# Kernel optimization log

Hardware: AMD Instinct MI355X
Metric: run time of the kernel (lower is better)

Reference implementation:

```python
import jax, jax.numpy as jnp
import numpy as np

B, T, C, H, D = 128, 256, 384, 6, 64  # batch, seq (block_size), embed, heads, head_size


def setup_inputs() -> dict:
    key = jax.random.key(0)
    ks = jax.random.split(key, 6)
    s = 0.02  # init scale
    return {
        "x": jax.random.normal(ks[0], (B, T, C), dtype=jnp.float32),
        "wq": jax.random.normal(ks[1], (H, C, D), dtype=jnp.float32) * s,
        "wk": jax.random.normal(ks[2], (H, C, D), dtype=jnp.float32) * s,
        "wv": jax.random.normal(ks[3], (H, C, D), dtype=jnp.float32) * s,
        "wp": jax.random.normal(ks[4], (H * D, C), dtype=jnp.float32) * s,
        "bp": jax.random.normal(ks[5], (C,), dtype=jnp.float32) * s,
    }


def reference(x, wq, wk, wv, wp, bp):
    # Batched multi-head causal self-attention (eval mode: dropout = identity).
    Bx, Tx, Cx = x.shape
    q = jnp.einsum("btc,hcd->bhtd", x, wq)
    k = jnp.einsum("btc,hcd->bhtd", x, wk)
    v = jnp.einsum("btc,hcd->bhtd", x, wv)
    scale = jnp.asarray(D, x.dtype) ** -0.5
    scores = jnp.einsum("bhtd,bhsd->bhts", q, k) * scale
    mask = jnp.tril(jnp.ones((Tx, Tx), dtype=bool))  # causal
    scores = jnp.where(mask, scores, -jnp.inf)
    w = jax.nn.softmax(scores, axis=-1)
    out = jnp.einsum("bhts,bhsd->bhtd", w, v)
    out = out.transpose(0, 2, 1, 3).reshape(Bx, Tx, H * D)  # concat heads
    return out @ wp + bp
```

## Files before the change

kernel.cpp:

```cpp
#include <hip/hip_runtime.h>
#include <hip/hip_bf16.h>

typedef __bf16 bf16x8 __attribute__((ext_vector_type(8)));
typedef __bf16 bf16x4 __attribute__((ext_vector_type(4)));
typedef float  f32x4  __attribute__((ext_vector_type(4)));

#define MFMA16(a,b,c) __builtin_amdgcn_mfma_f32_16x16x32_bf16((a),(b),(c),0,0,0)

static constexpr int Tt = 256;
static constexpr int Cc = 384;
static constexpr int Hh = 6;
static constexpr int Dd = 64;
static constexpr int HD = 384;
static constexpr int NQ = 1152;

__global__ __launch_bounds__(256) void prep_w(
    const float* __restrict__ wq, const float* __restrict__ wk,
    const float* __restrict__ wv, const float* __restrict__ wp,
    __bf16* __restrict__ wqkvb, __bf16* __restrict__ wpb)
{
  int idx = blockIdx.x * 256 + threadIdx.x;
  const int n1 = NQ * Cc;
  if (idx < n1) {
    int n = idx / Cc, c = idx % Cc;
    int which = n / HD, r = n % HD, h = r >> 6, d = r & 63;
    const float* w = which == 0 ? wq : (which == 1 ? wk : wv);
    wqkvb[idx] = (__bf16)w[(h * Cc + c) * Dd + d];
  } else {
    int j = idx - n1;
    if (j < Cc * HD) {
      int co = j / HD, ci = j % HD;
      wpb[j] = (__bf16)wp[ci * Cc + co];
    }
  }
}

__global__ __launch_bounds__(256) void gemm_qkv(
    const float* __restrict__ x, const __bf16* __restrict__ wn,
    __bf16* __restrict__ qkv, int Mc)
{
  __shared__ __align__(16) char smem[36864];
  __bf16* Al = (__bf16*)smem;
  __bf16* Bl = (__bf16*)(smem + 18432);

  const int tid = threadIdx.x;
  const int m0 = blockIdx.x * 128;
  const int n0 = blockIdx.y * 128;
  const int wid = tid >> 6, lane = tid & 63;
  const int wm = wid >> 1, wn_ = wid & 1;
  const int lr = lane & 15, lg = lane >> 4;

  f32x4 acc[4][4];
#pragma unroll
  for (int i = 0; i < 4; ++i)
#pragma unroll
    for (int j = 0; j < 4; ++j) acc[i][j] = f32x4{0.f, 0.f, 0.f, 0.f};

  for (int kt = 0; kt < Cc; kt += 64) {
#pragma unroll
    for (int i = 0; i < 8; ++i) {
      int idx = tid + 256 * i;
      int row = idx >> 4, c4 = idx & 15;
      float4 v = *(const float4*)(x + (size_t)(m0 + row) * Cc + kt + c4 * 4);
      bf16x4 b; b[0] = (__bf16)v.x; b[1] = (__bf16)v.y; b[2] = (__bf16)v.z; b[3] = (__bf16)v.w;
      *(bf16x4*)((char*)Al + row * 144 + c4 * 8) = b;
    }
#pragma unroll
    for (int i = 0; i < 4; ++i) {
      int idx = tid + 256 * i;
      int row = idx >> 3, k8 = idx & 7;
      bf16x8 v = *(const bf16x8*)(wn + (size_t)(n0 + row) * Cc + kt + k8 * 8);
      *(bf16x8*)((char*)Bl + row * 144 + k8 * 16) = v;
    }
    __syncthreads();
#pragma unroll
    for (int ks = 0; ks < 2; ++ks) {
      bf16x8 af[4], bfr[4];
#pragma unroll
      for (int mi = 0; mi < 4; ++mi)
        af[mi] = *(const bf16x8*)((char*)Al + (wm * 64 + mi * 16 + lr) * 144 + ks * 64 + lg * 16);
#pragma unroll
      for (int ni = 0; ni < 4; ++ni)
        bfr[ni] = *(const bf16x8*)((char*)Bl + (wn_ * 64 + ni * 16 + lr) * 144 + ks * 64 + lg * 16);
#pragma unroll
      for (int mi = 0; mi < 4; ++mi)
#pragma unroll
        for (int ni = 0; ni < 4; ++ni)
          acc[mi][ni] = MFMA16(af[mi], bfr[ni], acc[mi][ni]);
    }
    __syncthreads();
  }

  __bf16* Cl = (__bf16*)smem;
#pragma unroll
  for (int mi = 0; mi < 4; ++mi)
#pragma unroll
    for (int ni = 0; ni < 4; ++ni)
#pragma unroll
      for (int j = 0; j < 4; ++j) {
        int row = wm * 64 + mi * 16 + lg * 4 + j;
        int col = wn_ * 64 + ni * 16 + lr;
        *((__bf16*)((char*)Cl + row * 272 + col * 2)) = (__bf16)acc[mi][ni][j];
      }
  __syncthreads();
#pragma unroll
  for (int p = 0; p < 8; ++p) {
    int row = p * 16 + (tid >> 4);
    int ch = tid & 15;
    bf16x8 v = *(const bf16x8*)((char*)Cl + row * 272 + ch * 16);
    int m = m0 + row, n = n0 + ch * 8;
    int which = n / HD, r = n % HD, h = r >> 6, d = r & 63;
    int bl = m >> 8, t = m & 255;
    *(bf16x8*)(qkv + (size_t)which * ((size_t)Mc * HD) +
               ((size_t)(bl * Hh + h) * Tt + t) * Dd + d) = v;
  }
}

__global__ __launch_bounds__(256) void attn_k(
    const __bf16* __restrict__ q, const __bf16* __restrict__ k,
    const __bf16* __restrict__ v, __bf16* __restrict__ att)
{
  __shared__ __align__(16) char smem[98304];
  char* Kl = smem;
  char* Vl = smem + 32768;
  char* Pl = smem + 65536;

  const int bh = blockIdx.x;
  const int tid = threadIdx.x, wid = tid >> 6, lane = tid & 63;
  const int lr = lane & 15, lg = lane >> 4;
  const size_t base = (size_t)bh * (Tt * Dd);

#pragma unroll
  for (int i = 0; i < 8; ++i) {
    int chunk = tid + 256 * i;
    int key = chunk >> 3, d8 = chunk & 7;
    bf16x8 kv = *(const bf16x8*)(k + base + key * 64 + d8 * 8);
    *(bf16x8*)(Kl + ((key * 128 + d8 * 16) ^ ((key & 7) << 4))) = kv;
  }
#pragma unroll
  for (int i = 0; i < 8; ++i) {
    int chunk = tid + 256 * i;
    int key = chunk >> 3, d8 = chunk & 7;
    bf16x8 vv = *(const bf16x8*)(v + base + key * 64 + d8 * 8);
#pragma unroll
    for (int e = 0; e < 8; ++e) {
      int d = d8 * 8 + e;
      *(__bf16*)(Vl + ((d * 512 + key * 2) ^ ((d & 7) << 4))) = vv[e];
    }
  }
  __syncthreads();

  char* Pw = Pl + wid * 8192;
  const int bl = bh / Hh, h = bh % Hh;

  for (int qi = 0; qi < 4; ++qi) {
    const int qt = wid + qi * 4;
    const int qbase = qt * 16;

    bf16x8 qf0 = *(const bf16x8*)(q + base + (qbase + lr) * 64 + lg * 8);
    bf16x8 qf1 = *(const bf16x8*)(q + base + (qbase + lr) * 64 + 32 + lg * 8);

    f32x4 s[16];
#pragma unroll
    for (int n = 0; n < 16; ++n) s[n] = f32x4{0.f, 0.f, 0.f, 0.f};
#pragma unroll
    for (int n = 0; n < 16; ++n) {
      if (n <= qt) {
        int rowb = (n * 16 + lr) * 128;
        int swz = (lr & 7) << 4;
        bf16x8 k0 = *(const bf16x8*)(Kl + ((rowb + lg * 16) ^ swz));
        bf16x8 k1 = *(const bf16x8*)(Kl + ((rowb + 64 + lg * 16) ^ swz));
        s[n] = MFMA16(qf0, k0, s[n]);
        s[n] = MFMA16(qf1, k1, s[n]);
      }
    }
#pragma unroll
    for (int n = 0; n < 16; ++n)
#pragma unroll
      for (int j = 0; j < 4; ++j) {
        int key = n * 16 + lr;
        int qrow = qbase + lg * 4 + j;
        s[n][j] = (n <= qt && key <= qrow) ? s[n][j] * 0.125f : -1e30f;
      }
    float m4[4] = {-1e30f, -1e30f, -1e30f, -1e30f};
#pragma unroll
    for (int n = 0; n < 16; ++n)
#pragma unroll
      for (int j = 0; j < 4; ++j) m4[j] = fmaxf(m4[j], s[n][j]);
#pragma unroll
    for (int j = 0; j < 4; ++j) {
      m4[j] = fmaxf(m4[j], __shfl_xor(m4[j], 1));
      m4[j] = fmaxf(m4[j], __shfl_xor(m4[j], 2));
      m4[j] = fmaxf(m4[j], __shfl_xor(m4[j], 4));
      m4[j] = fmaxf(m4[j], __shfl_xor(m4[j], 8));
    }
    float sum4[4] = {0.f, 0.f, 0.f, 0.f};
#pragma unroll
    for (int n = 0; n < 16; ++n)
#pragma unroll
      for (int j = 0; j < 4; ++j) {
        float p = __expf(s[n][j] - m4[j]);
        s[n][j] = p;
        sum4[j] += p;
      }
#pragma unroll
    for (int j = 0; j < 4; ++j) {
      sum4[j] += __shfl_xor(sum4[j], 1);
      sum4[j] += __shfl_xor(sum4[j], 2);
      sum4[j] += __shfl_xor(sum4[j], 4);
      sum4[j] += __shfl_xor(sum4[j], 8);
    }
    float inv4[4];
#pragma unroll
    for (int j = 0; j < 4; ++j) inv4[j] = 1.0f / sum4[j];

#pragma unroll
    for (int j = 0; j < 4; ++j) {
      int ql = lg * 4 + j;
      int rswz = (ql & 7) << 4;
#pragma unroll
      for (int n = 0; n < 16; ++n) {
        float p = s[n][j] * inv4[j];
        *(__bf16*)(Pw + ((ql * 512 + (n * 16 + lr) * 2) ^ rswz)) = (__bf16)p;
      }
    }
    asm volatile("s_waitcnt lgkmcnt(0)" ::: "memory");

    f32x4 o[4];
#pragma unroll
    for (int dn = 0; dn < 4; ++dn) o[dn] = f32x4{0.f, 0.f, 0.f, 0.f};
    const int kkmax = (qbase + 15) >> 5;
#pragma unroll
    for (int kk = 0; kk < 8; ++kk) {
      if (kk <= kkmax) {
        bf16x8 pa = *(const bf16x8*)(Pw + ((lr * 512 + kk * 64 + lg * 16) ^ ((lr & 7) << 4)));
#pragma unroll
        for (int dn = 0; dn < 4; ++dn) {
          int d = dn * 16 + lr;
          bf16x8 vb = *(const bf16x8*)(Vl + ((d * 512 + kk * 64 + lg * 16) ^ ((d & 7) << 4)));
          o[dn] = MFMA16(pa, vb, o[dn]);
        }
      }
    }
#pragma unroll
    for (int dn = 0; dn < 4; ++dn)
#pragma unroll
      for (int j = 0; j < 4; ++j) {
        int qrow = qbase + lg * 4 + j;
        att[((size_t)(bl * Tt + qrow)) * HD + h * Dd + dn * 16 + lr] = (__bf16)o[dn][j];
      }
  }
}

__global__ __launch_bounds__(256) void gemm_out(
    const __bf16* __restrict__ att, const __bf16* __restrict__ wpb,
    const float* __restrict__ bp, float* __restrict__ out, int Mc)
{
  __shared__ __align__(16) char smem[36864];
  __bf16* Al = (__bf16*)smem;
  __bf16* Bl = (__bf16*)(smem + 18432);

  const int tid = threadIdx.x;
  const int m0 = blockIdx.x * 128;
  const int n0 = blockIdx.y * 128;
  const int wid = tid >> 6, lane = tid & 63;
  const int wm = wid >> 1, wn_ = wid & 1;
  const int lr = lane & 15, lg = lane >> 4;

  f32x4 acc[4][4];
#pragma unroll
  for (int i = 0; i < 4; ++i)
#pragma unroll
    for (int j = 0; j < 4; ++j) acc[i][j] = f32x4{0.f, 0.f, 0.f, 0.f};

  for (int kt = 0; kt < Cc; kt += 64) {
#pragma unroll
    for (int i = 0; i < 4; ++i) {
      int idx = tid + 256 * i;
      int row = idx >> 3, k8 = idx & 7;
      bf16x8 v = *(const bf16x8*)(att + (size_t)(m0 + row) * Cc + kt + k8 * 8);
      *(bf16x8*)((char*)Al + row * 144 + k8 * 16) = v;
    }
#pragma unroll
    for (int i = 0; i < 4; ++i) {
      int idx = tid + 256 * i;
      int row = idx >> 3, k8 = idx & 7;
      bf16x8 v = *(const bf16x8*)(wpb + (size_t)(n0 + row) * Cc + kt + k8 * 8);
      *(bf16x8*)((char*)Bl + row * 144 + k8 * 16) = v;
    }
    __syncthreads();
#pragma unroll
    for (int ks = 0; ks < 2; ++ks) {
      bf16x8 af[4], bfr[4];
#pragma unroll
      for (int mi = 0; mi < 4; ++mi)
        af[mi] = *(const bf16x8*)((char*)Al + (wm * 64 + mi * 16 + lr) * 144 + ks * 64 + lg * 16);
#pragma unroll
      for (int ni = 0; ni < 4; ++ni)
        bfr[ni] = *(const bf16x8*)((char*)Bl + (wn_ * 64 + ni * 16 + lr) * 144 + ks * 64 + lg * 16);
#pragma unroll
      for (int mi = 0; mi < 4; ++mi)
#pragma unroll
        for (int ni = 0; ni < 4; ++ni)
          acc[mi][ni] = MFMA16(af[mi], bfr[ni], acc[mi][ni]);
    }
    __syncthreads();
  }
#pragma unroll
  for (int ni = 0; ni < 4; ++ni) {
    int n = n0 + wn_ * 64 + ni * 16 + lr;
    float bv = bp[n];
#pragma unroll
    for (int mi = 0; mi < 4; ++mi)
#pragma unroll
      for (int j = 0; j < 4; ++j) {
        int m = m0 + wm * 64 + mi * 16 + lg * 4 + j;
        out[(size_t)m * Cc + n] = acc[mi][ni][j] + bv;
      }
  }
}

extern "C" void kernel_launch(void* const* d_in, const int* in_sizes, int n_in,
                              void* d_out, int out_size, void* d_ws, size_t ws_size,
                              hipStream_t stream) {
  const float* x  = (const float*)d_in[0];
  const float* wq = (const float*)d_in[1];
  const float* wk = (const float*)d_in[2];
  const float* wv = (const float*)d_in[3];
  const float* wp = (const float*)d_in[4];
  const float* bp = (const float*)d_in[5];
  float* out = (float*)d_out;

  char* ws = (char*)d_ws;
  __bf16* wqkvb = (__bf16*)ws;
  __bf16* wpb   = (__bf16*)(ws + 884736);
  char*   dyn   = ws + 1179648;

  int Bc = 128;
  while (Bc > 1 && 1179648ull + (unsigned long long)Bc * 786432ull > (unsigned long long)ws_size)
    Bc >>= 1;
  const int Mc = Bc * 256;
  __bf16* qkv = (__bf16*)dyn;
  __bf16* att = (__bf16*)(dyn + (size_t)3 * Mc * HD * 2);

  prep_w<<<2304, 256, 0, stream>>>(wq, wk, wv, wp, wqkvb, wpb);

  for (int b0 = 0; b0 < 128; b0 += Bc) {
    const float* xc  = x + (size_t)b0 * Tt * Cc;
    float* outc      = out + (size_t)b0 * Tt * Cc;
    gemm_qkv<<<dim3(Mc / 128, 9), 256, 0, stream>>>(xc, wqkvb, qkv, Mc);
    attn_k<<<Bc * Hh, 256, 0, stream>>>(qkv, qkv + (size_t)Mc * HD,
                                        qkv + (size_t)2 * Mc * HD, att);
    gemm_out<<<dim3(Mc / 128, 3), 256, 0, stream>>>(att, wpb, bp, outc, Mc);
  }
}
```

Baseline: 253.6 us.

## Use direct global-to-LDS loads, pre-cast x, widen attention blocks to 512 threads

Adds a separate kernel that casts x to bf16 once, so both GEMMs can stage tiles with global_load_lds into XOR-swizzled LDS in place of padded register round-trips. Attention now runs 8 waves per block with balanced causal query-tile pairing (wid and 15-wid), and loads K via direct LDS loads. s_setprio brackets the MFMA sections. The xb buffer is aliased with att to save workspace. This adds an extra kernel launch and a bf16 round-trip of x through memory, and raises LDS use in attention to 128 KB.

```diff
diff --git a/kernel.cpp b/kernel.cpp
--- a/kernel.cpp
+++ b/kernel.cpp
@@ -13,6 +13,24 @@
 static constexpr int Dd = 64;
 static constexpr int HD = 384;
 static constexpr int NQ = 1152;
+
+__device__ __forceinline__ void gload16(const void* g, void* l) {
+  __builtin_amdgcn_global_load_lds(
+      (const __attribute__((address_space(1))) void*)g,
+      (__attribute__((address_space(3))) void*)l, 16, 0, 0);
+}
+
+__global__ __launch_bounds__(256) void xcast(
+    const float* __restrict__ x, __bf16* __restrict__ xb)
+{
+  size_t i = (size_t)blockIdx.x * 256 + threadIdx.x;
+  const float4* p = (const float4*)(x + i * 8);
+  float4 a = p[0], b = p[1];
+  bf16x8 o;
+  o[0] = (__bf16)a.x; o[1] = (__bf16)a.y; o[2] = (__bf16)a.z; o[3] = (__bf16)a.w;
+  o[4] = (__bf16)b.x; o[5] = (__bf16)b.y; o[6] = (__bf16)b.z; o[7] = (__bf16)b.w;
+  *(bf16x8*)(xb + i * 8) = o;
+}
 
 __global__ __launch_bounds__(256) void prep_w(
     const float* __restrict__ wq, const float* __restrict__ wk,
@@ -36,19 +54,20 @@
 }
 
 __global__ __launch_bounds__(256) void gemm_qkv(
-    const float* __restrict__ x, const __bf16* __restrict__ wn,
+    const __bf16* __restrict__ xb, const __bf16* __restrict__ wn,
     __bf16* __restrict__ qkv, int Mc)
 {
   __shared__ __align__(16) char smem[36864];
-  __bf16* Al = (__bf16*)smem;
-  __bf16* Bl = (__bf16*)(smem + 18432);
+  char* Al = smem;
+  char* Bl = smem + 16384;
 
   const int tid = threadIdx.x;
   const int m0 = blockIdx.x * 128;
   const int n0 = blockIdx.y * 128;
-  const int wid = tid >> 6, lane = tid & 63;
+  const int wid = tid >> 6, ln = tid & 63;
   const int wm = wid >> 1, wn_ = wid & 1;
-  const int lr = lane & 15, lg = lane >> 4;
+  const int lr = ln & 15, lg = ln >> 4;
+  const int srow = ln >> 3, sslot = ln & 7;
 
   f32x4 acc[4][4];
 #pragma unroll
@@ -58,35 +77,38 @@
 
   for (int kt = 0; kt < Cc; kt += 64) {
 #pragma unroll
-    for (int i = 0; i < 8; ++i) {
-      int idx = tid + 256 * i;
-      int row = idx >> 4, c4 = idx & 15;
-      float4 v = *(const float4*)(x + (size_t)(m0 + row) * Cc + kt + c4 * 4);
-      bf16x4 b; b[0] = (__bf16)v.x; b[1] = (__bf16)v.y; b[2] = (__bf16)v.z; b[3] = (__bf16)v.w;
-      *(bf16x4*)((char*)Al + row * 144 + c4 * 8) = b;
-    }
-#pragma unroll
     for (int i = 0; i < 4; ++i) {
-      int idx = tid + 256 * i;
-      int row = idx >> 3, k8 = idx & 7;
-      bf16x8 v = *(const bf16x8*)(wn + (size_t)(n0 + row) * Cc + kt + k8 * 8);
-      *(bf16x8*)((char*)Bl + row * 144 + k8 * 16) = v;
+      int off = (wid * 4 + i) << 10;
+      int row = (off >> 7) + srow;
+      gload16(xb + (size_t)(m0 + row) * Cc + kt + ((sslot ^ (row & 7)) << 3), Al + off);
+    }
+#pragma unroll
+    for (int i = 0; i < 4; ++i) {
+      int off = (wid * 4 + i) << 10;
+      int row = (off >> 7) + srow;
+      gload16(wn + (size_t)(n0 + row) * Cc + kt + ((sslot ^ (row & 7)) << 3), Bl + off);
     }
     __syncthreads();
 #pragma unroll
     for (int ks = 0; ks < 2; ++ks) {
       bf16x8 af[4], bfr[4];
 #pragma unroll
-      for (int mi = 0; mi < 4; ++mi)
-        af[mi] = *(const bf16x8*)((char*)Al + (wm * 64 + mi * 16 + lr) * 144 + ks * 64 + lg * 16);
-#pragma unroll
-      for (int ni = 0; ni < 4; ++ni)
-        bfr[ni] = *(const bf16x8*)((char*)Bl + (wn_ * 64 + ni * 16 + lr) * 144 + ks * 64 + lg * 16);
+      for (int mi = 0; mi < 4; ++mi) {
+        int r = wm * 64 + mi * 16 + lr;
+        af[mi] = *(const bf16x8*)(Al + r * 128 + (((ks * 4 + lg) ^ (r & 7)) << 4));
+      }
+#pragma unroll
+      for (int ni = 0; ni < 4; ++ni) {
+        int r = wn_ * 64 + ni * 16 + lr;
+        bfr[ni] = *(const bf16x8*)(Bl + r * 128 + (((ks * 4 + lg) ^ (r & 7)) << 4));
+      }
+      __builtin_amdgcn_s_setprio(1);
 #pragma unroll
       for (int mi = 0; mi < 4; ++mi)
 #pragma unroll
         for (int ni = 0; ni < 4; ++ni)
           acc[mi][ni] = MFMA16(af[mi], bfr[ni], acc[mi][ni]);
+      __builtin_amdgcn_s_setprio(0);
     }
     __syncthreads();
   }
@@ -116,11 +138,11 @@
   }
 }
 
-__global__ __launch_bounds__(256) void attn_k(
+__global__ __launch_bounds__(512) void attn_k(
     const __bf16* __restrict__ q, const __bf16* __restrict__ k,
     const __bf16* __restrict__ v, __bf16* __restrict__ att)
 {
-  __shared__ __align__(16) char smem[98304];
+  __shared__ __align__(16) char smem[131072];
   char* Kl = smem;
   char* Vl = smem + 32768;
   char* Pl = smem + 65536;
@@ -131,15 +153,15 @@
   const size_t base = (size_t)bh * (Tt * Dd);
 
 #pragma unroll
-  for (int i = 0; i < 8; ++i) {
-    int chunk = tid + 256 * i;
-    int key = chunk >> 3, d8 = chunk & 7;
-    bf16x8 kv = *(const bf16x8*)(k + base + key * 64 + d8 * 8);
-    *(bf16x8*)(Kl + ((key * 128 + d8 * 16) ^ ((key & 7) << 4))) = kv;
-  }
-#pragma unroll
-  for (int i = 0; i < 8; ++i) {
-    int chunk = tid + 256 * i;
+  for (int i = 0; i < 4; ++i) {
+    int off = (wid * 4 + i) << 10;
+    int row = (off >> 7) + (lane >> 3);
+    int slot = lane & 7;
+    gload16(k + base + row * 64 + ((slot ^ (row & 7)) << 3), Kl + off);
+  }
+#pragma unroll
+  for (int i = 0; i < 4; ++i) {
+    int chunk = tid + 512 * i;
     int key = chunk >> 3, d8 = chunk & 7;
     bf16x8 vv = *(const bf16x8*)(v + base + key * 64 + d8 * 8);
 #pragma unroll
@@ -153,8 +175,8 @@
   char* Pw = Pl + wid * 8192;
   const int bl = bh / Hh, h = bh % Hh;
 
-  for (int qi = 0; qi < 4; ++qi) {
-    const int qt = wid + qi * 4;
+  for (int qi = 0; qi < 2; ++qi) {
+    const int qt = qi == 0 ? wid : 15 - wid;
     const int qbase = qt * 16;
 
     bf16x8 qf0 = *(const bf16x8*)(q + base + (qbase + lr) * 64 + lg * 8);
@@ -163,6 +185,7 @@
     f32x4 s[16];
 #pragma unroll
     for (int n = 0; n < 16; ++n) s[n] = f32x4{0.f, 0.f, 0.f, 0.f};
+    __builtin_amdgcn_s_setprio(1);
 #pragma unroll
     for (int n = 0; n < 16; ++n) {
       if (n <= qt) {
@@ -174,6 +197,7 @@
         s[n] = MFMA16(qf1, k1, s[n]);
       }
     }
+    __builtin_amdgcn_s_setprio(0);
 #pragma unroll
     for (int n = 0; n < 16; ++n)
 #pragma unroll
@@ -230,6 +254,7 @@
 #pragma unroll
     for (int dn = 0; dn < 4; ++dn) o[dn] = f32x4{0.f, 0.f, 0.f, 0.f};
     const int kkmax = (qbase + 15) >> 5;
+    __builtin_amdgcn_s_setprio(1);
 #pragma unroll
     for (int kk = 0; kk < 8; ++kk) {
       if (kk <= kkmax) {
@@ -242,6 +267,7 @@
         }
       }
     }
+    __builtin_amdgcn_s_setprio(0);
 #pragma unroll
     for (int dn = 0; dn < 4; ++dn)
 #pragma unroll
@@ -256,16 +282,17 @@
     const __bf16* __restrict__ att, const __bf16* __restrict__ wpb,
     const float* __restrict__ bp, float* __restrict__ out, int Mc)
 {
-  __shared__ __align__(16) char smem[36864];
-  __bf16* Al = (__bf16*)smem;
-  __bf16* Bl = (__bf16*)(smem + 18432);
+  __shared__ __align__(16) char smem[32768];
+  char* Al = smem;
+  char* Bl = smem + 16384;
 
   const int tid = threadIdx.x;
   const int m0 = blockIdx.x * 128;
   const int n0 = blockIdx.y * 128;
-  const int wid = tid >> 6, lane = tid & 63;
+  const int wid = tid >> 6, ln = tid & 63;
   const int wm = wid >> 1, wn_ = wid & 1;
-  const int lr = lane & 15, lg = lane >> 4;
+  const int lr = ln & 15, lg = ln >> 4;
+  const int srow = ln >> 3, sslot = ln & 7;
 
   f32x4 acc[4][4];
 #pragma unroll
@@ -276,33 +303,37 @@
   for (int kt = 0; kt < Cc; kt += 64) {
 #pragma unroll
     for (int i = 0; i < 4; ++i) {
-      int idx = tid + 256 * i;
-      int row = idx >> 3, k8 = idx & 7;
-      bf16x8 v = *(const bf16x8*)(att + (size_t)(m0 + row) * Cc + kt + k8 * 8);
-      *(bf16x8*)((char*)Al + row * 144 + k8 * 16) = v;
+      int off = (wid * 4 + i) << 10;
+      int row = (off >> 7) + srow;
+      gload16(att + (size_t)(m0 + row) * Cc + kt + ((sslot ^ (row & 7)) << 3), Al + off);
     }
 #pragma unroll
     for (int i = 0; i < 4; ++i) {
-      int idx = tid + 256 * i;
-      int row = idx >> 3, k8 = idx & 7;
-      bf16x8 v = *(const bf16x8*)(wpb + (size_t)(n0 + row) * Cc + kt + k8 * 8);
-      *(bf16x8*)((char*)Bl + row * 144 + k8 * 16) = v;
+      int off = (wid * 4 + i) << 10;
+      int row = (off >> 7) + srow;
+      gload16(wpb + (size_t)(n0 + row) * Cc + kt + ((sslot ^ (row & 7)) << 3), Bl + off);
     }
     __syncthreads();
 #pragma unroll
     for (int ks = 0; ks < 2; ++ks) {
       bf16x8 af[4], bfr[4];
 #pragma unroll
-      for (int mi = 0; mi < 4; ++mi)
-        af[mi] = *(const bf16x8*)((char*)Al + (wm * 64 + mi * 16 + lr) * 144 + ks * 64 + lg * 16);
-#pragma unroll
-      for (int ni = 0; ni < 4; ++ni)
-        bfr[ni] = *(const bf16x8*)((char*)Bl + (wn_ * 64 + ni * 16 + lr) * 144 + ks * 64 + lg * 16);
+      for (int mi = 0; mi < 4; ++mi) {
+        int r = wm * 64 + mi * 16 + lr;
+        af[mi] = *(const bf16x8*)(Al + r * 128 + (((ks * 4 + lg) ^ (r & 7)) << 4));
+      }
+#pragma unroll
+      for (int ni = 0; ni < 4; ++ni) {
+        int r = wn_ * 64 + ni * 16 + lr;
+        bfr[ni] = *(const bf16x8*)(Bl + r * 128 + (((ks * 4 + lg) ^ (r & 7)) << 4));
+      }
+      __builtin_amdgcn_s_setprio(1);
 #pragma unroll
       for (int mi = 0; mi < 4; ++mi)
 #pragma unroll
         for (int ni = 0; ni < 4; ++ni)
           acc[mi][ni] = MFMA16(af[mi], bfr[ni], acc[mi][ni]);
+      __builtin_amdgcn_s_setprio(0);
     }
     __syncthreads();
   }
@@ -340,16 +371,18 @@
   while (Bc > 1 && 1179648ull + (unsigned long long)Bc * 786432ull > (unsigned long long)ws_size)
     Bc >>= 1;
   const int Mc = Bc * 256;
-  __bf16* qkv = (__bf16*)dyn;
-  __bf16* att = (__bf16*)(dyn + (size_t)3 * Mc * HD * 2);
+  __bf16* xb  = (__bf16*)dyn;
+  __bf16* att = xb;
+  __bf16* qkv = (__bf16*)(dyn + (size_t)Mc * HD * 2);
 
   prep_w<<<2304, 256, 0, stream>>>(wq, wk, wv, wp, wqkvb, wpb);
 
   for (int b0 = 0; b0 < 128; b0 += Bc) {
     const float* xc  = x + (size_t)b0 * Tt * Cc;
     float* outc      = out + (size_t)b0 * Tt * Cc;
-    gemm_qkv<<<dim3(Mc / 128, 9), 256, 0, stream>>>(xc, wqkvb, qkv, Mc);
-    attn_k<<<Bc * Hh, 256, 0, stream>>>(qkv, qkv + (size_t)Mc * HD,
+    xcast<<<Bc * 48, 256, 0, stream>>>(xc, xb);
+    gemm_qkv<<<dim3(Mc / 128, 9), 256, 0, stream>>>(xb, wqkvb, qkv, Mc);
+    attn_k<<<Bc * Hh, 512, 0, stream>>>(qkv, qkv + (size_t)Mc * HD,
                                         qkv + (size_t)2 * Mc * HD, att);
     gemm_out<<<dim3(Mc / 128, 3), 256, 0, stream>>>(att, wpb, bp, outc, Mc);
   }
```

Result: faster. 218.5 us (-13.9%).
